# Optimization experiments

Measured on AMD Instinct MI355X. Metric: run time of the kernel, lower is better.

## Reference

```python
import jax, jax.numpy as jnp
import numpy as np

N_TOKENS = 4096   # flattened batch*seq tokens
D_MODEL = 1024
N_EXPERT = 8
D_HIDDEN = 1024   # expert FFN hidden size
TOP_K = 2


def setup_inputs() -> dict:
    key = jax.random.key(0)
    ks = jax.random.split(key, 4)
    f32 = jnp.float32
    return {
        "inp": jax.random.normal(ks[0], (N_TOKENS, D_MODEL), f32),
        "gate_w": jax.random.normal(ks[1], (D_MODEL, N_EXPERT), f32) * 0.02,
        "gate_b": jnp.zeros((N_EXPERT,), f32),
        "w1": jax.random.normal(ks[2], (N_EXPERT, D_MODEL, D_HIDDEN), f32) * 0.02,
        "b1": jnp.zeros((N_EXPERT, D_HIDDEN), f32),
        "w2": jax.random.normal(ks[3], (N_EXPERT, D_HIDDEN, D_MODEL), f32) * 0.02,
        "b2": jnp.zeros((N_EXPERT, D_MODEL), f32),
    }


def reference(inp, gate_w, gate_b, w1, b1, w2, b2):
    """FMoE forward: NaiveGate top-k -> dispatch -> per-expert FFN -> weighted combine.

    Math is identical to dispatch/grouped-GEMM/gather: since both top-k slots of a
    token see the same input, out[n] = sum_e coeff[n,e] * expert_e(inp[n]) where
    coeff[n,e] = sum_k softmax(top_vals)[n,k] * 1[top_idx[n,k] == e].
    """
    n_expert = gate_w.shape[-1]
    # NaiveGate: linear gate, top-k, softmax over the k selected logits
    logits = inp @ gate_w + gate_b                      # [N, E]
    top_val, top_idx = jax.lax.top_k(logits, TOP_K)     # [N, K]
    score = jax.nn.softmax(top_val, axis=-1)            # [N, K]
    # combine weights per (token, expert); top-k indices are distinct per token
    coeff = jnp.sum(
        jax.nn.one_hot(top_idx, n_expert, dtype=inp.dtype) * score[..., None],
        axis=1,
    )                                                   # [N, E]
    # expert FFN (exact-erf GeLU, matching torch.nn.functional.gelu)
    h = jax.nn.gelu(jnp.einsum('nd,edh->neh', inp, w1) + b1, approximate=False)  # [N, E, H]
    out = jnp.einsum('neh,ehd->nd', h * coeff[:, :, None], w2) + coeff @ b2      # [N, D]
    return out


if __name__ == "__main__":
    out = reference(**setup_inputs())
    print(out.shape, out.dtype)
```

## Files before the change

kernel.cpp:

```cpp
#include <hip/hip_runtime.h>
#include <math.h>

#define N_TOKENS 4096
#define D_MODEL  1024
#define N_EXPERT 8
#define D_HIDDEN 1024
#define N_POS    8192

typedef __bf16 bf16x8 __attribute__((ext_vector_type(8)));
typedef float  f32x4  __attribute__((ext_vector_type(4)));
typedef unsigned short u16x8 __attribute__((ext_vector_type(8)));

#define GLOBAL_AS __attribute__((address_space(1)))
#define LDS_AS    __attribute__((address_space(3)))

static __device__ __forceinline__ void async_ld16(const void* g, void* l) {
    __builtin_amdgcn_global_load_lds((GLOBAL_AS void*)g, (LDS_AS void*)l, 16, 0, 0);
}

static __device__ __forceinline__ unsigned short f2bf(float f) {
    unsigned int u = __builtin_bit_cast(unsigned int, f);
    u += 0x7fffu + ((u >> 16) & 1u);
    return (unsigned short)(u >> 16);
}
static __device__ __forceinline__ unsigned int pack2(float a, float b) {
    return (unsigned int)f2bf(a) | ((unsigned int)f2bf(b) << 16);
}
static __device__ __forceinline__ float bflo(unsigned int u) {
    return __builtin_bit_cast(float, u << 16);
}
static __device__ __forceinline__ float bfhi(unsigned int u) {
    return __builtin_bit_cast(float, u & 0xffff0000u);
}

__global__ __launch_bounds__(256) void convert_kernel(
    const float* __restrict__ w1, const float* __restrict__ w2,
    const float* __restrict__ inp,
    unsigned short* __restrict__ w1b, unsigned short* __restrict__ w2b,
    unsigned short* __restrict__ inp_bf, int* __restrict__ cnts)
{
    int tid = threadIdx.x;
    if (blockIdx.x == 0 && blockIdx.y == 0 && blockIdx.z == 0 && tid < 8)
        cnts[tid] = 0;
    int mat = blockIdx.z;
    int r0 = blockIdx.x * 64, c0 = blockIdx.y * 64;

    if (mat >= 16) {
        const float* src = inp + (size_t)(mat - 16) * 1048576;
        unsigned short* dst = inp_bf + (size_t)(mat - 16) * 1048576;
        #pragma unroll
        for (int i = 0; i < 4; ++i) {
            int r = (tid >> 4) + i * 16;
            float4 v = *(const float4*)(src + (size_t)(r0 + r) * 1024 + c0 + (tid & 15) * 4);
            uint2 u; u.x = pack2(v.x, v.y); u.y = pack2(v.z, v.w);
            *(uint2*)(dst + (size_t)(r0 + r) * 1024 + c0 + (tid & 15) * 4) = u;
        }
        return;
    }

    const float* src = (mat < 8) ? (w1 + (size_t)mat * 1048576)
                                 : (w2 + (size_t)(mat - 8) * 1048576);
    unsigned short* dst = (mat < 8) ? (w1b + (size_t)mat * 1048576)
                                    : (w2b + (size_t)(mat - 8) * 1048576);
    __shared__ float tile[64][68];
    #pragma unroll
    for (int i = 0; i < 4; ++i) {
        int r = (tid >> 4) + i * 16;
        float4 v = *(const float4*)(src + (size_t)(r0 + r) * 1024 + c0 + (tid & 15) * 4);
        *(float4*)&tile[r][(tid & 15) * 4] = v;
    }
    __syncthreads();
    int dr = tid >> 2;
    #pragma unroll
    for (int p = 0; p < 2; ++p) {
        int ch = (tid & 3) + p * 4;
        u16x8 o;
        #pragma unroll
        for (int j = 0; j < 8; ++j) o[j] = f2bf(tile[ch * 8 + j][dr]);
        *(u16x8*)(dst + (size_t)(c0 + dr) * 1024 + r0 + ch * 8) = o;
    }
}

__global__ __launch_bounds__(256) void gate_kernel(
    const float* __restrict__ inp, const float* __restrict__ gate_w,
    const float* __restrict__ gate_b, int* __restrict__ cnts,
    int* __restrict__ emeta, float* __restrict__ stok)
{
    __shared__ int bcnt[8], base[8];
    __shared__ int tinfo[16];
    int tid = threadIdx.x, lane = tid & 63, wave = tid >> 6;
    if (tid < 8) bcnt[tid] = 0;
    __syncthreads();

    for (int t = 0; t < 4; ++t) {
        int ti = wave * 4 + t;
        int n  = blockIdx.x * 16 + ti;
        const float* ip = inp + (size_t)n * D_MODEL;
        float acc[8] = {0.f,0.f,0.f,0.f,0.f,0.f,0.f,0.f};
        for (int d0 = lane * 4; d0 < D_MODEL; d0 += 256) {
            float4 x = *(const float4*)(ip + d0);
            #pragma unroll
            for (int j = 0; j < 4; ++j) {
                float xv = (j == 0) ? x.x : (j == 1) ? x.y : (j == 2) ? x.z : x.w;
                float4 g0 = *(const float4*)(gate_w + (d0 + j) * 8);
                float4 g1 = *(const float4*)(gate_w + (d0 + j) * 8 + 4);
                acc[0] += xv * g0.x; acc[1] += xv * g0.y;
                acc[2] += xv * g0.z; acc[3] += xv * g0.w;
                acc[4] += xv * g1.x; acc[5] += xv * g1.y;
                acc[6] += xv * g1.z; acc[7] += xv * g1.w;
            }
        }
        #pragma unroll
        for (int off = 32; off > 0; off >>= 1)
            #pragma unroll
            for (int e = 0; e < 8; ++e)
                acc[e] += __shfl_xor(acc[e], off, 64);
        #pragma unroll
        for (int e = 0; e < 8; ++e) acc[e] += gate_b[e];

        int e0 = 0; float v0 = acc[0];
        #pragma unroll
        for (int e = 1; e < 8; ++e) if (acc[e] > v0) { v0 = acc[e]; e0 = e; }
        int e1 = -1; float v1 = -1e30f;
        #pragma unroll
        for (int e = 0; e < 8; ++e) if (e != e0 && acc[e] > v1) { v1 = acc[e]; e1 = e; }
        float tv = expf(v1 - v0);
        float s0 = 1.0f / (1.0f + tv);
        float s1 = tv / (1.0f + tv);

        if (lane == 0) {
            int r0 = atomicAdd(&bcnt[e0], 1);
            int r1 = atomicAdd(&bcnt[e1], 1);
            tinfo[ti] = e0 | (e1 << 4) | (r0 << 8) | (r1 << 20);
            stok[2 * n]     = s0;
            stok[2 * n + 1] = s1;
        }
    }
    __syncthreads();
    if (tid < 8) base[tid] = atomicAdd(&cnts[tid], bcnt[tid]);
    __syncthreads();
    if (tid < 16) {
        int n = blockIdx.x * 16 + tid;
        unsigned int inf = (unsigned int)tinfo[tid];
        int e0 = inf & 15, e1 = (inf >> 4) & 15;
        int p0 = base[e0] + ((inf >> 8) & 4095);
        int p1 = base[e1] + (int)(inf >> 20);
        emeta[n] = e0 | (e1 << 4) | (p0 << 8) | (p1 << 20);
    }
}

__global__ __launch_bounds__(256) void plan_kernel(
    const int* __restrict__ cnts, const int* __restrict__ emeta,
    int* __restrict__ pos2tok)
{
    int n = blockIdx.x * 256 + threadIdx.x;
    unsigned int em = (unsigned int)emeta[n];
    int e0 = em & 15, e1 = (em >> 4) & 15;
    int p0 = (em >> 8) & 4095, p1 = (int)(em >> 20);
    int off0 = 0, off1 = 0;
    #pragma unroll
    for (int e = 0; e < 8; ++e) {
        int c = cnts[e];
        off0 += (e < e0) ? c : 0;
        off1 += (e < e1) ? c : 0;
    }
    pos2tok[off0 + p0] = n;
    pos2tok[off1 + p1] = n;
}

__global__ __launch_bounds__(256, 4) void ffn1_kernel(
    const unsigned short* __restrict__ inp_bf, const unsigned short* __restrict__ w1b,
    const float* __restrict__ b1, const int* __restrict__ cnts,
    const int* __restrict__ pos2tok, unsigned short* __restrict__ Hg)
{
    int bid = blockIdx.x;
    int e = bid & 7, nt = (bid >> 3) & 15, mt = bid >> 7;
    int off = 0, Ne = 0;
    #pragma unroll
    for (int i = 0; i < 8; ++i) {
        int c = cnts[i];
        off += (i < e) ? c : 0;
        Ne = (i == e) ? c : Ne;
    }
    int m0 = mt * 128;
    if (m0 >= Ne) return;
    int n0 = nt * 64;

    __shared__ unsigned short As[2 * 128 * 32];
    __shared__ unsigned short Bs[2 * 64 * 32];
    __shared__ int rowtok[128];

    int tid = threadIdx.x, lane = tid & 63, wave = tid >> 6;
    int lrow = lane >> 2, lchunk = lane & 3;
    int csw8 = (lchunk ^ ((lrow >> 1) & 3)) * 8;

    if (tid < 128) {
        int r = m0 + tid;
        if (r >= Ne) r = Ne - 1;
        rowtok[tid] = pos2tok[off + r];
    }
    __syncthreads();

    const unsigned short* aS0 =
        inp_bf + (size_t)rowtok[wave * 32 + lrow] * D_MODEL + csw8;
    const unsigned short* aS1 =
        inp_bf + (size_t)rowtok[wave * 32 + 16 + lrow] * D_MODEL + csw8;
    const unsigned short* bS = w1b + (size_t)e * D_MODEL * D_HIDDEN
                             + (size_t)(n0 + wave * 16 + lrow) * D_MODEL + csw8;
    unsigned short* aD0 = &As[(wave * 32) * 32];
    unsigned short* aD1 = &As[(wave * 32 + 16) * 32];
    unsigned short* bD  = &Bs[(wave * 16) * 32];

    f32x4 acc[4][2] = {};
    int wm = (wave & 1) * 64, wn = ((wave >> 1) & 1) * 32;
    int lane15 = lane & 15, quad = lane >> 4;
    int fro = (quad ^ ((lane15 >> 1) & 3)) * 8;

    for (int k0 = 0; k0 < D_MODEL; k0 += 64) {
        #pragma unroll
        for (int h = 0; h < 2; ++h) {
            int ko = k0 + h * 32;
            async_ld16(aS0 + ko, aD0 + h * 4096);
            async_ld16(aS1 + ko, aD1 + h * 4096);
            async_ld16(bS  + ko, bD  + h * 2048);
        }
        __syncthreads();
        #pragma unroll
        for (int h = 0; h < 2; ++h) {
            bf16x8 af[4], bf[2];
            #pragma unroll
            for (int t = 0; t < 4; ++t)
                af[t] = *(const bf16x8*)&As[h * 4096 + (wm + t * 16 + lane15) * 32 + fro];
            #pragma unroll
            for (int t = 0; t < 2; ++t)
                bf[t] = *(const bf16x8*)&Bs[h * 2048 + (wn + t * 16 + lane15) * 32 + fro];
            #pragma unroll
            for (int i = 0; i < 4; ++i)
                #pragma unroll
                for (int j = 0; j < 2; ++j)
                    acc[i][j] = __builtin_amdgcn_mfma_f32_16x16x32_bf16(
                        af[i], bf[j], acc[i][j], 0, 0, 0);
        }
        if (k0 + 64 < D_MODEL) __syncthreads();
    }

    const float* bexp = b1 + (size_t)e * D_HIDDEN;
    #pragma unroll
    for (int j = 0; j < 2; ++j) {
        int gcol = n0 + wn + j * 16 + lane15;
        float bv = bexp[gcol];
        #pragma unroll
        for (int i = 0; i < 4; ++i) {
            int rowb = wm + i * 16 + quad * 4;
            #pragma unroll
            for (int r = 0; r < 4; ++r) {
                int row = rowb + r;
                if (m0 + row < Ne) {
                    float x = acc[i][j][r] + bv;
                    float gv = 0.5f * x * (1.0f + erff(x * 0.70710678118654752f));
                    Hg[(size_t)(off + m0 + row) * D_HIDDEN + gcol] = f2bf(gv);
                }
            }
        }
    }
}

__global__ __launch_bounds__(256, 4) void ffn2_kernel(
    const unsigned short* __restrict__ Hg, const unsigned short* __restrict__ w2b,
    const int* __restrict__ cnts, unsigned short* __restrict__ Og)
{
    int bid = blockIdx.x;
    int e = bid & 7, nt = (bid >> 3) & 15, mt = bid >> 7;
    int off = 0, Ne = 0;
    #pragma unroll
    for (int i = 0; i < 8; ++i) {
        int c = cnts[i];
        off += (i < e) ? c : 0;
        Ne = (i == e) ? c : Ne;
    }
    int m0 = mt * 128;
    if (m0 >= Ne) return;
    int n0 = nt * 64;

    __shared__ unsigned short As[2 * 128 * 32];
    __shared__ unsigned short Bs[2 * 64 * 32];

    int tid = threadIdx.x, lane = tid & 63, wave = tid >> 6;
    int lrow = lane >> 2, lchunk = lane & 3;
    int csw8 = (lchunk ^ ((lrow >> 1) & 3)) * 8;

    int ga0 = off + m0 + wave * 32 + lrow;
    int ga1 = ga0 + 16;
    if (ga0 >= N_POS) ga0 = N_POS - 1;
    if (ga1 >= N_POS) ga1 = N_POS - 1;
    const unsigned short* aS0 = Hg + (size_t)ga0 * D_HIDDEN + csw8;
    const unsigned short* aS1 = Hg + (size_t)ga1 * D_HIDDEN + csw8;
    const unsigned short* bS = w2b + (size_t)e * D_HIDDEN * D_MODEL
                             + (size_t)(n0 + wave * 16 + lrow) * D_HIDDEN + csw8;
    unsigned short* aD0 = &As[(wave * 32) * 32];
    unsigned short* aD1 = &As[(wave * 32 + 16) * 32];
    unsigned short* bD  = &Bs[(wave * 16) * 32];

    f32x4 acc[4][2] = {};
    int wm = (wave & 1) * 64, wn = ((wave >> 1) & 1) * 32;
    int lane15 = lane & 15, quad = lane >> 4;
    int fro = (quad ^ ((lane15 >> 1) & 3)) * 8;

    for (int k0 = 0; k0 < D_HIDDEN; k0 += 64) {
        #pragma unroll
        for (int h = 0; h < 2; ++h) {
            int ko = k0 + h * 32;
            async_ld16(aS0 + ko, aD0 + h * 4096);
            async_ld16(aS1 + ko, aD1 + h * 4096);
            async_ld16(bS  + ko, bD  + h * 2048);
        }
        __syncthreads();
        #pragma unroll
        for (int h = 0; h < 2; ++h) {
            bf16x8 af[4], bf[2];
            #pragma unroll
            for (int t = 0; t < 4; ++t)
                af[t] = *(const bf16x8*)&As[h * 4096 + (wm + t * 16 + lane15) * 32 + fro];
            #pragma unroll
            for (int t = 0; t < 2; ++t)
                bf[t] = *(const bf16x8*)&Bs[h * 2048 + (wn + t * 16 + lane15) * 32 + fro];
            #pragma unroll
            for (int i = 0; i < 4; ++i)
                #pragma unroll
                for (int j = 0; j < 2; ++j)
                    acc[i][j] = __builtin_amdgcn_mfma_f32_16x16x32_bf16(
                        af[i], bf[j], acc[i][j], 0, 0, 0);
        }
        if (k0 + 64 < D_HIDDEN) __syncthreads();
    }

    #pragma unroll
    for (int j = 0; j < 2; ++j) {
        int gcol = n0 + wn + j * 16 + lane15;
        #pragma unroll
        for (int i = 0; i < 4; ++i) {
            int rowb = wm + i * 16 + quad * 4;
            #pragma unroll
            for (int r = 0; r < 4; ++r) {
                int row = rowb + r;
                if (m0 + row < Ne) {
                    Og[(size_t)(off + m0 + row) * D_MODEL + gcol] =
                        f2bf(acc[i][j][r]);
                }
            }
        }
    }
}

__global__ __launch_bounds__(256) void combine_kernel(
    const unsigned short* __restrict__ Og, const int* __restrict__ cnts,
    const int* __restrict__ emeta, const float* __restrict__ stok,
    const float* __restrict__ b2, float* __restrict__ out)
{
    int lane = threadIdx.x & 63, wave = threadIdx.x >> 6;
    int n = blockIdx.x * 4 + wave;
    unsigned int em = (unsigned int)emeta[n];
    int e0 = em & 15, e1 = (em >> 4) & 15;
    int p0 = (em >> 8) & 4095, p1 = (int)(em >> 20);
    int off0 = 0, off1 = 0;
    #pragma unroll
    for (int e = 0; e < 8; ++e) {
        int c = cnts[e];
        off0 += (e < e0) ? c : 0;
        off1 += (e < e1) ? c : 0;
    }
    int pos0 = off0 + p0, pos1 = off1 + p1;
    float s0 = stok[2 * n], s1 = stok[2 * n + 1];
    const unsigned short* o0 = Og + (size_t)pos0 * D_MODEL;
    const unsigned short* o1 = Og + (size_t)pos1 * D_MODEL;
    const float* bA = b2 + (size_t)e0 * D_MODEL;
    const float* bB = b2 + (size_t)e1 * D_MODEL;
    float* op = out + (size_t)n * D_MODEL;
    for (int d = lane * 4; d < D_MODEL; d += 256) {
        uint2 u0 = *(const uint2*)(o0 + d);
        uint2 u1 = *(const uint2*)(o1 + d);
        float4 xa = *(const float4*)(bA + d);
        float4 xb = *(const float4*)(bB + d);
        float4 r;
        r.x = s0 * (bflo(u0.x) + xa.x) + s1 * (bflo(u1.x) + xb.x);
        r.y = s0 * (bfhi(u0.x) + xa.y) + s1 * (bfhi(u1.x) + xb.y);
        r.z = s0 * (bflo(u0.y) + xa.z) + s1 * (bflo(u1.y) + xb.z);
        r.w = s0 * (bfhi(u0.y) + xa.w) + s1 * (bfhi(u1.y) + xb.w);
        *(float4*)(op + d) = r;
    }
}

extern "C" void kernel_launch(void* const* d_in, const int* in_sizes, int n_in,
                              void* d_out, int out_size, void* d_ws, size_t ws_size,
                              hipStream_t stream) {
    const float* inp    = (const float*)d_in[0];
    const float* gate_w = (const float*)d_in[1];
    const float* gate_b = (const float*)d_in[2];
    const float* w1     = (const float*)d_in[3];
    const float* b1     = (const float*)d_in[4];
    const float* w2     = (const float*)d_in[5];
    const float* b2     = (const float*)d_in[6];
    float* out = (float*)d_out;

    char* ws = (char*)d_ws;
    int*   cnts    = (int*)  (ws);
    int*   emeta   = (int*)  (ws + 4096);
    float* stok    = (float*)(ws + 65536);
    int*   pos2tok = (int*)  (ws + 131072);
    unsigned short* w2b = (unsigned short*)(ws + 1048576);
    unsigned short* Hg  = (unsigned short*)(ws + 17825792);
    unsigned short* w1b = (unsigned short*)(ws + 34603008);
    unsigned short* Og  = (unsigned short*)(ws + 34603008);

    unsigned short* inp_bf = (unsigned short*)d_out;

    convert_kernel<<<dim3(16, 16, 20), 256, 0, stream>>>(
        w1, w2, inp, w1b, w2b, inp_bf, cnts);
    gate_kernel<<<dim3(N_TOKENS / 16), 256, 0, stream>>>(
        inp, gate_w, gate_b, cnts, emeta, stok);
    plan_kernel<<<dim3(N_TOKENS / 256), 256, 0, stream>>>(cnts, emeta, pos2tok);
    ffn1_kernel<<<dim3(4096), 256, 0, stream>>>(
        inp_bf, w1b, b1, cnts, pos2tok, Hg);
    ffn2_kernel<<<dim3(4096), 256, 0, stream>>>(Hg, w2b, cnts, Og);
    combine_kernel<<<dim3(N_TOKENS / 4), 256, 0, stream>>>(
        Og, cnts, emeta, stok, b2, out);
}
```

Before: 224.5 us.

## Fuse gate/plan into convert kernel and scatter-add ffn2 output into result

```diff
diff --git a/kernel.cpp b/kernel.cpp
--- a/kernel.cpp
+++ b/kernel.cpp
@@ -26,75 +26,70 @@
 static __device__ __forceinline__ unsigned int pack2(float a, float b) {
     return (unsigned int)f2bf(a) | ((unsigned int)f2bf(b) << 16);
 }
-static __device__ __forceinline__ float bflo(unsigned int u) {
-    return __builtin_bit_cast(float, u << 16);
-}
-static __device__ __forceinline__ float bfhi(unsigned int u) {
-    return __builtin_bit_cast(float, u & 0xffff0000u);
-}
-
-__global__ __launch_bounds__(256) void convert_kernel(
-    const float* __restrict__ w1, const float* __restrict__ w2,
-    const float* __restrict__ inp,
+
+__global__ __launch_bounds__(256) void prep_kernel(
+    const float* __restrict__ inp, const float* __restrict__ gate_w,
+    const float* __restrict__ gate_b, const float* __restrict__ w1,
+    const float* __restrict__ w2,
     unsigned short* __restrict__ w1b, unsigned short* __restrict__ w2b,
-    unsigned short* __restrict__ inp_bf, int* __restrict__ cnts)
+    unsigned short* __restrict__ inp_bf,
+    int* __restrict__ gcnt, int* __restrict__ emeta, float* __restrict__ stok,
+    int* __restrict__ cnts, int* __restrict__ pos2tok,
+    float* __restrict__ pos_score, int* __restrict__ done)
 {
-    int tid = threadIdx.x;
-    if (blockIdx.x == 0 && blockIdx.y == 0 && blockIdx.z == 0 && tid < 8)
-        cnts[tid] = 0;
-    int mat = blockIdx.z;
-    int r0 = blockIdx.x * 64, c0 = blockIdx.y * 64;
-
-    if (mat >= 16) {
-        const float* src = inp + (size_t)(mat - 16) * 1048576;
-        unsigned short* dst = inp_bf + (size_t)(mat - 16) * 1048576;
-        #pragma unroll
-        for (int i = 0; i < 4; ++i) {
-            int r = (tid >> 4) + i * 16;
-            float4 v = *(const float4*)(src + (size_t)(r0 + r) * 1024 + c0 + (tid & 15) * 4);
-            uint2 u; u.x = pack2(v.x, v.y); u.y = pack2(v.z, v.w);
-            *(uint2*)(dst + (size_t)(r0 + r) * 1024 + c0 + (tid & 15) * 4) = u;
+    __shared__ __align__(16) char smem[17408];
+    int job = blockIdx.x, tid = threadIdx.x;
+
+    if (job >= 256) {
+        int cj = job - 256;
+        int mat = cj >> 8, t = cj & 255;
+        int r0 = (t & 15) * 64, c0 = (t >> 4) * 64;
+        if (mat >= 16) {
+            const float* src = inp + (size_t)(mat - 16) * 1048576;
+            unsigned short* dst = inp_bf + (size_t)(mat - 16) * 1048576;
+            #pragma unroll
+            for (int i = 0; i < 4; ++i) {
+                int r = (tid >> 4) + i * 16;
+                float4 v = *(const float4*)(src + (size_t)(r0 + r) * 1024
+                                            + c0 + (tid & 15) * 4);
+                uint2 u; u.x = pack2(v.x, v.y); u.y = pack2(v.z, v.w);
+                *(uint2*)(dst + (size_t)(r0 + r) * 1024 + c0 + (tid & 15) * 4) = u;
+            }
+        } else {
+            const float* src = (mat < 8) ? (w1 + (size_t)mat * 1048576)
+                                         : (w2 + (size_t)(mat - 8) * 1048576);
+            unsigned short* dst = (mat < 8) ? (w1b + (size_t)mat * 1048576)
+                                            : (w2b + (size_t)(mat - 8) * 1048576);
+            float (*tile)[68] = (float(*)[68])smem;
+            #pragma unroll
+            for (int i = 0; i < 4; ++i) {
+                int r = (tid >> 4) + i * 16;
+                float4 v = *(const float4*)(src + (size_t)(r0 + r) * 1024
+                                            + c0 + (tid & 15) * 4);
+                *(float4*)&tile[r][(tid & 15) * 4] = v;
+            }
+            __syncthreads();
+            int dr = tid >> 2;
+            #pragma unroll
+            for (int p = 0; p < 2; ++p) {
+                int ch = (tid & 3) + p * 4;
+                u16x8 o;
+                #pragma unroll
+                for (int j = 0; j < 8; ++j) o[j] = f2bf(tile[ch * 8 + j][dr]);
+                *(u16x8*)(dst + (size_t)(c0 + dr) * 1024 + r0 + ch * 8) = o;
+            }
         }
         return;
     }
 
-    const float* src = (mat < 8) ? (w1 + (size_t)mat * 1048576)
-                                 : (w2 + (size_t)(mat - 8) * 1048576);
-    unsigned short* dst = (mat < 8) ? (w1b + (size_t)mat * 1048576)
-                                    : (w2b + (size_t)(mat - 8) * 1048576);
-    __shared__ float tile[64][68];
-    #pragma unroll
-    for (int i = 0; i < 4; ++i) {
-        int r = (tid >> 4) + i * 16;
-        float4 v = *(const float4*)(src + (size_t)(r0 + r) * 1024 + c0 + (tid & 15) * 4);
-        *(float4*)&tile[r][(tid & 15) * 4] = v;
-    }
-    __syncthreads();
-    int dr = tid >> 2;
-    #pragma unroll
-    for (int p = 0; p < 2; ++p) {
-        int ch = (tid & 3) + p * 4;
-        u16x8 o;
-        #pragma unroll
-        for (int j = 0; j < 8; ++j) o[j] = f2bf(tile[ch * 8 + j][dr]);
-        *(u16x8*)(dst + (size_t)(c0 + dr) * 1024 + r0 + ch * 8) = o;
-    }
-}
-
-__global__ __launch_bounds__(256) void gate_kernel(
-    const float* __restrict__ inp, const float* __restrict__ gate_w,
-    const float* __restrict__ gate_b, int* __restrict__ cnts,
-    int* __restrict__ emeta, float* __restrict__ stok)
-{
-    __shared__ int bcnt[8], base[8];
-    __shared__ int tinfo[16];
-    int tid = threadIdx.x, lane = tid & 63, wave = tid >> 6;
+    __shared__ int bcnt[8], tinfo[16], isLast;
+    int lane = tid & 63, wave = tid >> 6;
+    int g = job;
     if (tid < 8) bcnt[tid] = 0;
     __syncthreads();
-
     for (int t = 0; t < 4; ++t) {
         int ti = wave * 4 + t;
-        int n  = blockIdx.x * 16 + ti;
+        int n  = g * 16 + ti;
         const float* ip = inp + (size_t)n * D_MODEL;
         float acc[8] = {0.f,0.f,0.f,0.f,0.f,0.f,0.f,0.f};
         for (int d0 = lane * 4; d0 < D_MODEL; d0 += 256) {
@@ -123,11 +118,11 @@
         for (int e = 1; e < 8; ++e) if (acc[e] > v0) { v0 = acc[e]; e0 = e; }
         int e1 = -1; float v1 = -1e30f;
         #pragma unroll
-        for (int e = 0; e < 8; ++e) if (e != e0 && acc[e] > v1) { v1 = acc[e]; e1 = e; }
+        for (int e = 0; e < 8; ++e)
+            if (e != e0 && acc[e] > v1) { v1 = acc[e]; e1 = e; }
         float tv = expf(v1 - v0);
         float s0 = 1.0f / (1.0f + tv);
         float s1 = tv / (1.0f + tv);
-
         if (lane == 0) {
             int r0 = atomicAdd(&bcnt[e0], 1);
             int r1 = atomicAdd(&bcnt[e1], 1);
@@ -137,35 +132,51 @@
         }
     }
     __syncthreads();
-    if (tid < 8) base[tid] = atomicAdd(&cnts[tid], bcnt[tid]);
-    __syncthreads();
-    if (tid < 16) {
-        int n = blockIdx.x * 16 + tid;
-        unsigned int inf = (unsigned int)tinfo[tid];
-        int e0 = inf & 15, e1 = (inf >> 4) & 15;
-        int p0 = base[e0] + ((inf >> 8) & 4095);
-        int p1 = base[e1] + (int)(inf >> 20);
-        emeta[n] = e0 | (e1 << 4) | (p0 << 8) | (p1 << 20);
-    }
-}
-
-__global__ __launch_bounds__(256) void plan_kernel(
-    const int* __restrict__ cnts, const int* __restrict__ emeta,
-    int* __restrict__ pos2tok)
-{
-    int n = blockIdx.x * 256 + threadIdx.x;
-    unsigned int em = (unsigned int)emeta[n];
-    int e0 = em & 15, e1 = (em >> 4) & 15;
-    int p0 = (em >> 8) & 4095, p1 = (int)(em >> 20);
-    int off0 = 0, off1 = 0;
-    #pragma unroll
-    for (int e = 0; e < 8; ++e) {
-        int c = cnts[e];
-        off0 += (e < e0) ? c : 0;
-        off1 += (e < e1) ? c : 0;
-    }
-    pos2tok[off0 + p0] = n;
-    pos2tok[off1 + p1] = n;
+    if (tid < 8)  gcnt[g * 8 + tid]   = bcnt[tid];
+    if (tid < 16) emeta[g * 16 + tid] = tinfo[tid];
+    __syncthreads();
+    if (tid == 0) {
+        __threadfence();
+        isLast = (atomicAdd(done, 1) == 255);
+    }
+    __syncthreads();
+    if (!isLast) return;
+    __threadfence();
+
+    int* lc  = (int*)smem;
+    int* lb  = lc + 2048;
+    int* lex = lb + 2048;
+    for (int i = tid; i < 2048; i += 256) lc[i] = gcnt[i];
+    __syncthreads();
+    if (tid < 8) {
+        int run = 0;
+        for (int q = 0; q < 256; ++q) {
+            lb[q * 8 + tid] = run;
+            run += lc[q * 8 + tid];
+        }
+        lex[8 + tid] = run;
+        cnts[tid] = run;
+    }
+    __syncthreads();
+    if (tid == 0) {
+        int o = 0;
+        #pragma unroll
+        for (int e = 0; e < 8; ++e) { lex[e] = o; o += lex[8 + e]; }
+    }
+    __syncthreads();
+    {
+        int q = tid;
+        for (int ti = 0; ti < 16; ++ti) {
+            int n = q * 16 + ti;
+            unsigned int em = (unsigned int)emeta[n];
+            int e0 = em & 15, e1 = (em >> 4) & 15;
+            int r0 = (em >> 8) & 4095, r1 = (int)(em >> 20);
+            int pos0 = lex[e0] + lb[q * 8 + e0] + r0;
+            int pos1 = lex[e1] + lb[q * 8 + e1] + r1;
+            pos2tok[pos0] = n;  pos_score[pos0] = stok[2 * n];
+            pos2tok[pos1] = n;  pos_score[pos1] = stok[2 * n + 1];
+        }
+    }
 }
 
 __global__ __launch_bounds__(256, 4) void ffn1_kernel(
@@ -267,7 +278,9 @@
 
 __global__ __launch_bounds__(256, 4) void ffn2_kernel(
     const unsigned short* __restrict__ Hg, const unsigned short* __restrict__ w2b,
-    const int* __restrict__ cnts, unsigned short* __restrict__ Og)
+    const int* __restrict__ cnts, const int* __restrict__ pos2tok,
+    const float* __restrict__ pos_score, const float* __restrict__ b2,
+    float* __restrict__ out)
 {
     int bid = blockIdx.x;
     int e = bid & 7, nt = (bid >> 3) & 15, mt = bid >> 7;
@@ -284,10 +297,20 @@
 
     __shared__ unsigned short As[2 * 128 * 32];
     __shared__ unsigned short Bs[2 * 64 * 32];
+    __shared__ int   rowtok[128];
+    __shared__ float psc[128];
 
     int tid = threadIdx.x, lane = tid & 63, wave = tid >> 6;
     int lrow = lane >> 2, lchunk = lane & 3;
     int csw8 = (lchunk ^ ((lrow >> 1) & 3)) * 8;
+
+    if (tid < 128) {
+        int r = m0 + tid;
+        if (r >= Ne) r = Ne - 1;
+        rowtok[tid] = pos2tok[off + r];
+        psc[tid]    = pos_score[off + r];
+    }
+    __syncthreads();
 
     int ga0 = off + m0 + wave * 32 + lrow;
     int ga1 = ga0 + 16;
@@ -334,9 +357,11 @@
         if (k0 + 64 < D_HIDDEN) __syncthreads();
     }
 
+    const float* b2e = b2 + (size_t)e * D_MODEL;
     #pragma unroll
     for (int j = 0; j < 2; ++j) {
         int gcol = n0 + wn + j * 16 + lane15;
+        float b2v = b2e[gcol];
         #pragma unroll
         for (int i = 0; i < 4; ++i) {
             int rowb = wm + i * 16 + quad * 4;
@@ -344,49 +369,11 @@
             for (int r = 0; r < 4; ++r) {
                 int row = rowb + r;
                 if (m0 + row < Ne) {
-                    Og[(size_t)(off + m0 + row) * D_MODEL + gcol] =
-                        f2bf(acc[i][j][r]);
+                    atomicAdd(&out[(size_t)rowtok[row] * D_MODEL + gcol],
+                              psc[row] * (acc[i][j][r] + b2v));
                 }
             }
         }
-    }
-}
-
-__global__ __launch_bounds__(256) void combine_kernel(
-    const unsigned short* __restrict__ Og, const int* __restrict__ cnts,
-    const int* __restrict__ emeta, const float* __restrict__ stok,
-    const float* __restrict__ b2, float* __restrict__ out)
-{
-    int lane = threadIdx.x & 63, wave = threadIdx.x >> 6;
-    int n = blockIdx.x * 4 + wave;
-    unsigned int em = (unsigned int)emeta[n];
-    int e0 = em & 15, e1 = (em >> 4) & 15;
-    int p0 = (em >> 8) & 4095, p1 = (int)(em >> 20);
-    int off0 = 0, off1 = 0;
-    #pragma unroll
-    for (int e = 0; e < 8; ++e) {
-        int c = cnts[e];
-        off0 += (e < e0) ? c : 0;
-        off1 += (e < e1) ? c : 0;
-    }
-    int pos0 = off0 + p0, pos1 = off1 + p1;
-    float s0 = stok[2 * n], s1 = stok[2 * n + 1];
-    const unsigned short* o0 = Og + (size_t)pos0 * D_MODEL;
-    const unsigned short* o1 = Og + (size_t)pos1 * D_MODEL;
-    const float* bA = b2 + (size_t)e0 * D_MODEL;
-    const float* bB = b2 + (size_t)e1 * D_MODEL;
-    float* op = out + (size_t)n * D_MODEL;
-    for (int d = lane * 4; d < D_MODEL; d += 256) {
-        uint2 u0 = *(const uint2*)(o0 + d);
-        uint2 u1 = *(const uint2*)(o1 + d);
-        float4 xa = *(const float4*)(bA + d);
-        float4 xb = *(const float4*)(bB + d);
-        float4 r;
-        r.x = s0 * (bflo(u0.x) + xa.x) + s1 * (bflo(u1.x) + xb.x);
-        r.y = s0 * (bfhi(u0.x) + xa.y) + s1 * (bfhi(u1.x) + xb.y);
-        r.z = s0 * (bflo(u0.y) + xa.z) + s1 * (bflo(u1.y) + xb.z);
-        r.w = s0 * (bfhi(u0.y) + xa.w) + s1 * (bfhi(u1.y) + xb.w);
-        *(float4*)(op + d) = r;
     }
 }
 
@@ -403,25 +390,26 @@
     float* out = (float*)d_out;
 
     char* ws = (char*)d_ws;
-    int*   cnts    = (int*)  (ws);
-    int*   emeta   = (int*)  (ws + 4096);
-    float* stok    = (float*)(ws + 65536);
-    int*   pos2tok = (int*)  (ws + 131072);
+    int*   cnts      = (int*)  (ws);
+    int*   done      = (int*)  (ws + 128);
+    int*   emeta     = (int*)  (ws + 4096);
+    float* stok      = (float*)(ws + 65536);
+    int*   pos2tok   = (int*)  (ws + 131072);
+    float* pos_score = (float*)(ws + 196608);
+    int*   gcnt      = (int*)  (ws + 262144);
     unsigned short* w2b = (unsigned short*)(ws + 1048576);
     unsigned short* Hg  = (unsigned short*)(ws + 17825792);
     unsigned short* w1b = (unsigned short*)(ws + 34603008);
-    unsigned short* Og  = (unsigned short*)(ws + 34603008);
 
     unsigned short* inp_bf = (unsigned short*)d_out;
 
-    convert_kernel<<<dim3(16, 16, 20), 256, 0, stream>>>(
-        w1, w2, inp, w1b, w2b, inp_bf, cnts);
-    gate_kernel<<<dim3(N_TOKENS / 16), 256, 0, stream>>>(
-        inp, gate_w, gate_b, cnts, emeta, stok);
-    plan_kernel<<<dim3(N_TOKENS / 256), 256, 0, stream>>>(cnts, emeta, pos2tok);
+    hipMemsetAsync(done, 0, sizeof(int), stream);
+    prep_kernel<<<dim3(5376), 256, 0, stream>>>(
+        inp, gate_w, gate_b, w1, w2, w1b, w2b, inp_bf,
+        gcnt, emeta, stok, cnts, pos2tok, pos_score, done);
     ffn1_kernel<<<dim3(4096), 256, 0, stream>>>(
         inp_bf, w1b, b1, cnts, pos2tok, Hg);
-    ffn2_kernel<<<dim3(4096), 256, 0, stream>>>(Hg, w2b, cnts, Og);
-    combine_kernel<<<dim3(N_TOKENS / 4), 256, 0, stream>>>(
-        Og, cnts, emeta, stok, b2, out);
-}
+    hipMemsetAsync(out, 0, (size_t)N_TOKENS * D_MODEL * sizeof(float), stream);
+    ffn2_kernel<<<dim3(4096), 256, 0, stream>>>(
+        Hg, w2b, cnts, pos2tok, pos_score, b2, out);
+}
```

Result: slower. 252.7 us (+12.6%).
